# Kernel tuning notes

Measured on AMD Instinct MI355X. Metric: run time of the kernel, lower is better.

The kernel has to match this reference:

```python
import jax, jax.numpy as jnp
import numpy as np

B, S, D = 4, 2048, 1024


def setup_inputs() -> dict:
    key = jax.random.key(0)
    ks = jax.random.split(key, 9)
    scale = 1.0 / np.sqrt(D)
    q = jax.random.normal(ks[0], (B, S, D), dtype=jnp.float32)
    k = jax.random.normal(ks[1], (B, S, D), dtype=jnp.float32)
    v = jax.random.normal(ks[2], (B, S, D), dtype=jnp.float32)
    w_q = jax.random.uniform(ks[3], (D, D), jnp.float32, -scale, scale)
    b_q = jax.random.uniform(ks[4], (D,), jnp.float32, -scale, scale)
    w_k = jax.random.uniform(ks[5], (D, D), jnp.float32, -scale, scale)
    b_k = jax.random.uniform(ks[6], (D,), jnp.float32, -scale, scale)
    w_v = jax.random.uniform(ks[7], (D, D), jnp.float32, -scale, scale)
    b_v = jax.random.uniform(ks[8], (D,), jnp.float32, -scale, scale)
    # additive causal mask: 0 on/below diagonal, -1e9 above
    causal = jnp.where(jnp.tril(jnp.ones((S, S), dtype=bool)), 0.0, -1e9)
    mask = causal[None, :, :].astype(jnp.float32)  # [1, S, S]
    return {"q": q, "k": k, "v": v, "mask": mask,
            "w_q": w_q, "b_q": b_q, "w_k": w_k, "b_k": b_k,
            "w_v": w_v, "b_v": b_v}


def reference(q, k, v, mask, w_q, b_q, w_k, b_k, w_v, b_v):
    # nn.Linear: x @ W^T + b
    query = jnp.einsum('bsd,ed->bse', q, w_q) + b_q  # [B,S,D]
    key_ = jnp.einsum('bsd,ed->bse', k, w_k) + b_k
    value = jnp.einsum('bsd,ed->bse', v, w_v) + b_v
    inv_sqrt_dk = 1.0 / jnp.sqrt(jnp.asarray(D, dtype=query.dtype))
    att = jnp.einsum('bqd,bkd->bqk', query, key_) * inv_sqrt_dk  # [B,S,S]
    att = att + mask
    score = jax.nn.softmax(att, axis=-1)
    return jnp.einsum('bqk,bkd->bqd', score, value)  # [B,S,D]
```

## Files before the change

### kernel.cpp

```cpp
#include <hip/hip_runtime.h>
#include <hip/hip_bf16.h>

#define SS 2048
#define DD 1024
#define NB 4

typedef __attribute__((ext_vector_type(8))) short  bf8;
typedef __attribute__((ext_vector_type(4))) float  f32x4;

static __device__ __forceinline__ unsigned short f2bf(float f) {
    unsigned u = __float_as_uint(f);
    u += 0x7fffu + ((u >> 16) & 1u);
    return (unsigned short)(u >> 16);
}
static __device__ __forceinline__ float bf2f(unsigned short u) {
    return __uint_as_float((unsigned)u << 16);
}
static __device__ __forceinline__ unsigned short f2bf_hw(float f) {
    union { __hip_bfloat16 h; unsigned short s; } u;
    u.h = __float2bfloat16(f);
    return u.s;
}

static __device__ __forceinline__ void gload_lds16(const void* g, void* lds) {
    __builtin_amdgcn_global_load_lds((__attribute__((address_space(1))) void*)g,
                                     (__attribute__((address_space(3))) void*)lds,
                                     16, 0, 0);
}

__global__ __launch_bounds__(256)
void cvt3(const float* __restrict__ a, const float* __restrict__ b, const float* __restrict__ c,
          unsigned short* __restrict__ oa, unsigned short* __restrict__ ob,
          unsigned short* __restrict__ oc, int n4) {
    int i = blockIdx.x * 256 + threadIdx.x;
    if (i >= n4) return;
    const float* in = blockIdx.y == 0 ? a : blockIdx.y == 1 ? b : c;
    unsigned short* out = blockIdx.y == 0 ? oa : blockIdx.y == 1 ? ob : oc;
    float4 v = ((const float4*)in)[i];
    ushort4 o;
    o.x = f2bf(v.x); o.y = f2bf(v.y); o.z = f2bf(v.z); o.w = f2bf(v.w);
    ((ushort4*)out)[i] = o;
}

#define BM 128
#define BN 128
#define BK 64

template<int MODE>
__global__ __launch_bounds__(256, 2)
void gemm_bt(const void* __restrict__ A0v, const unsigned short* __restrict__ B0p,
             const float* __restrict__ bias0,
             const void* __restrict__ A1v, const unsigned short* __restrict__ B1p,
             const float* __restrict__ bias1,
             const void* __restrict__ A2v, const unsigned short* __restrict__ B2p,
             const float* __restrict__ bias2,
             void* __restrict__ Cout)
{
    constexpr int LDA = (MODE == 3) ? 2048 : 1024;
    constexpr int LDB = (MODE == 3) ? 2048 : 1024;

    int bx, by, bz;
    if (MODE == 2) {
        int f  = (int)blockIdx.x;
        int f2 = (f & 7) * 68 + (f >> 3);
        bz = f2 / 136;
        int r = f2 - bz * 136;
        by = (int)((__fsqrt_rn(8.f * (float)r + 1.f) - 1.f) * 0.5f);
        if (by > 15) by = 15;
        while ((by + 1) * (by + 2) / 2 <= r) ++by;
        while (by * (by + 1) / 2 > r) --by;
        bx = r - by * (by + 1) / 2;
    } else {
        constexpr int GX  = 8;
        constexpr int NWG = (MODE == 0) ? 512 : 192;
        constexpr int CPX = NWG >> 3;
        int f  = (int)blockIdx.y * GX + (int)blockIdx.x;
        int f2 = (f & 7) * CPX + (f >> 3);
        bx = f2 % GX; by = f2 / GX;
        bz = blockIdx.z;
    }

    const float* Af = nullptr;
    const unsigned short* Ab = nullptr;
    const unsigned short* Bm;
    const float* bias = nullptr;
    int len, qt = 0, nsp = 1;
    if (MODE == 0) {
        Af   = ((const float*)(bz == 0 ? A0v : bz == 1 ? A1v : A2v)) + (size_t)by * BM * LDA;
        Bm   = (bz == 0 ? B0p : bz == 1 ? B1p : B2p) + (size_t)bx * BN * LDB;
        bias = bz == 0 ? bias0 : bz == 1 ? bias1 : bias2;
        len  = 1024;
    } else if (MODE == 2) {
        Ab  = (const unsigned short*)A0v + (size_t)bz * SS * DD + (size_t)by * BM * LDA;
        Bm  = B0p + (size_t)bz * SS * DD + (size_t)bx * BN * LDB;
        len = 1024;
    } else {
        int seg = 0;
        if (by < 8) { qt = by; nsp = 1; }
        else        { qt = 8 + ((by - 8) >> 1); seg = (by - 8) & 1; nsp = 2; }
        int ktot = (qt + 1) * 128, hk = ktot >> 1;
        int kst  = (nsp == 2 && seg) ? hk : 0;
        len = (nsp == 1) ? ktot : hk;
        Ab = (const unsigned short*)A0v + (size_t)bz * SS * SS + (size_t)qt * BM * LDA + kst;
        Bm = B0p + (size_t)bz * DD * SS + (size_t)bx * BN * LDB + kst;
    }

    constexpr int ABYTES = (MODE == 0) ? 32768 : 16384;
    __shared__ __align__(16) char AsB[ABYTES];
    __shared__ __align__(16) unsigned short Bs[BN * BK];

    const int t = threadIdx.x;
    const int l = t & 63;
    const int w = t >> 6;
    const int wr = w >> 1, wc = w & 1;

    const int srow0 = t >> 3;
    const int sswz  = (t & 7) ^ ((t >> 3) & 7);

    f32x4 zero = {0.f, 0.f, 0.f, 0.f};
    f32x4 acc[4][4];
    #pragma unroll
    for (int i = 0; i < 4; i++)
        #pragma unroll
        for (int j = 0; j < 4; j++) acc[i][j] = zero;

    const int ar = wr * 64 + (l & 15);
    const int br = wc * 64 + (l & 15);
    const int j0 = l >> 4;

    for (int kk = 0; kk < len; kk += BK) {
        if (MODE == 0) {
            #pragma unroll
            for (int j = 0; j < 8; ++j) {
                int seg = w * 8 + j;
                int r   = seg * 4 + (l >> 4);
                int sz  = ((r & 7) << 1) | ((r >> 3) & 1);
                int cg  = (l & 15) ^ sz;
                gload_lds16(Af + (size_t)r * LDA + kk + cg * 4,
                            AsB + (size_t)(seg * 64 + l) * 16);
            }
        } else {
            #pragma unroll
            for (int j = 0; j < 4; ++j) {
                int r = srow0 + 32 * j;
                gload_lds16(Ab + (size_t)r * LDA + kk + sswz * 8,
                            AsB + (t + 256 * j) * 16);
            }
        }
        #pragma unroll
        for (int j = 0; j < 4; ++j) {
            int r = srow0 + 32 * j;
            gload_lds16(Bm + (size_t)r * LDB + kk + sswz * 8,
                        (char*)Bs + (t + 256 * j) * 16);
        }
        __syncthreads();
        #pragma unroll
        for (int ks = 0; ks < 2; ++ks) {
            bf8 af[4], bfr[4];
            #pragma unroll
            for (int i = 0; i < 4; i++) {
                int r = ar + i * 16;
                if (MODE == 0) {
                    int sz = ((r & 7) << 1) | ((r >> 3) & 1);
                    int c0 = ks * 8 + j0 * 2;
                    const char* rowb = AsB + (size_t)r * 256;
                    f32x4 lo = *(const f32x4*)(rowb + ((c0)     ^ sz) * 16);
                    f32x4 hi = *(const f32x4*)(rowb + ((c0 + 1) ^ sz) * 16);
                    bf8 vv;
                    vv[0] = (short)f2bf_hw(lo[0]); vv[1] = (short)f2bf_hw(lo[1]);
                    vv[2] = (short)f2bf_hw(lo[2]); vv[3] = (short)f2bf_hw(lo[3]);
                    vv[4] = (short)f2bf_hw(hi[0]); vv[5] = (short)f2bf_hw(hi[1]);
                    vv[6] = (short)f2bf_hw(hi[2]); vv[7] = (short)f2bf_hw(hi[3]);
                    af[i] = vv;
                } else {
                    af[i] = *(const bf8*)(AsB + (size_t)r * 128 +
                                          (((j0 + ks * 4) ^ (r & 7)) << 4));
                }
            }
            #pragma unroll
            for (int j = 0; j < 4; j++) {
                int r = br + j * 16;
                bfr[j] = *(const bf8*)((char*)Bs + (size_t)r * 128 +
                                       (((j0 + ks * 4) ^ (r & 7)) << 4));
            }
            #pragma unroll
            for (int i = 0; i < 4; i++)
                #pragma unroll
                for (int j = 0; j < 4; j++)
                    acc[i][j] = __builtin_amdgcn_mfma_f32_16x16x32_bf16(af[i], bfr[j], acc[i][j], 0, 0, 0);
        }
        __syncthreads();
    }

    const int mb = ((MODE == 3) ? qt : by) * BM + wr * 64;
    const int nb = bx * BN + wc * 64;

    if (MODE == 0) {
        float bv[4];
        #pragma unroll
        for (int j = 0; j < 4; j++) bv[j] = bias[nb + j * 16 + (l & 15)];
        if (bz < 2) {
            unsigned short* C = (unsigned short*)Cout + (size_t)bz * NB * SS * DD;
            #pragma unroll
            for (int i = 0; i < 4; i++) {
                int m0 = mb + i * 16 + ((l >> 4) << 2);
                #pragma unroll
                for (int j = 0; j < 4; j++) {
                    int n = nb + j * 16 + (l & 15);
                    #pragma unroll
                    for (int r = 0; r < 4; r++)
                        C[(size_t)(m0 + r) * DD + n] = f2bf(acc[i][j][r] + bv[j]);
                }
            }
        } else {
            unsigned short* C = (unsigned short*)Cout + (size_t)2 * NB * SS * DD;
            int batch = (by * BM) >> 11;
            #pragma unroll
            for (int i = 0; i < 4; i++) {
                int s = (mb - batch * SS) + i * 16 + ((l >> 4) << 2);
                #pragma unroll
                for (int j = 0; j < 4; j++) {
                    int n = nb + j * 16 + (l & 15);
                    ushort4 pk;
                    pk.x = f2bf(acc[i][j][0] + bv[j]);
                    pk.y = f2bf(acc[i][j][1] + bv[j]);
                    pk.z = f2bf(acc[i][j][2] + bv[j]);
                    pk.w = f2bf(acc[i][j][3] + bv[j]);
                    *(ushort4*)&C[(size_t)batch * DD * SS + (size_t)n * SS + s] = pk;
                }
            }
        }
    } else if (MODE == 2) {
        unsigned short* C = (unsigned short*)Cout + (size_t)bz * SS * SS;
        #pragma unroll
        for (int i = 0; i < 4; i++) {
            int m0 = mb + i * 16 + ((l >> 4) << 2);
            #pragma unroll
            for (int j = 0; j < 4; j++) {
                int n = nb + j * 16 + (l & 15);
                #pragma unroll
                for (int r = 0; r < 4; r++)
                    C[(size_t)(m0 + r) * SS + n] = f2bf(acc[i][j][r] * 0.03125f);
            }
        }
    } else {
        float* C = (float*)Cout + (size_t)bz * SS * DD;
        #pragma unroll
        for (int i = 0; i < 4; i++) {
            int m0 = mb + i * 16 + ((l >> 4) << 2);
            #pragma unroll
            for (int j = 0; j < 4; j++) {
                int n = nb + j * 16 + (l & 15);
                if (nsp == 1) {
                    #pragma unroll
                    for (int r = 0; r < 4; r++)
                        C[(size_t)(m0 + r) * DD + n] = acc[i][j][r];
                } else {
                    #pragma unroll
                    for (int r = 0; r < 4; r++)
                        atomicAdd(&C[(size_t)(m0 + r) * DD + n], acc[i][j][r]);
                }
            }
        }
    }
}

__global__ __launch_bounds__(256)
void softmax_causal(const unsigned short* __restrict__ Sb, unsigned short* __restrict__ P) {
    __shared__ float tm[4], tl[4];
    int row = blockIdx.x;
    int b = row >> 11, q = row & 2047;
    const unsigned short* s = Sb + ((size_t)b * SS + q) * SS;
    unsigned short* p = P + ((size_t)b * SS + q) * SS;
    int len  = q + 1;
    int len8 = len >> 3;
    int wlen = ((q >> 7) + 1) << 7;

    float m = -3e38f, lsum = 0.f;
    for (int i8 = threadIdx.x; i8 < len8; i8 += 256) {
        ushort4 u0 = ((const ushort4*)s)[i8 * 2];
        ushort4 u1 = ((const ushort4*)s)[i8 * 2 + 1];
        float v[8] = {bf2f(u0.x), bf2f(u0.y), bf2f(u0.z), bf2f(u0.w),
                      bf2f(u1.x), bf2f(u1.y), bf2f(u1.z), bf2f(u1.w)};
        float cm = v[0];
        #pragma unroll
        for (int e = 1; e < 8; ++e) cm = fmaxf(cm, v[e]);
        float cs = 0.f;
        #pragma unroll
        for (int e = 0; e < 8; ++e) cs += __expf(v[e] - cm);
        float nm = fmaxf(m, cm);
        lsum = lsum * __expf(m - nm) + cs * __expf(cm - nm);
        m = nm;
    }
    for (int i = (len8 << 3) + threadIdx.x; i < len; i += 256) {
        float v = bf2f(s[i]);
        float nm = fmaxf(m, v);
        lsum = lsum * __expf(m - nm) + __expf(v - nm);
        m = nm;
    }
    #pragma unroll
    for (int o = 32; o; o >>= 1) {
        float om = __shfl_xor(m, o);
        float ol = __shfl_xor(lsum, o);
        float nm = fmaxf(m, om);
        lsum = lsum * __expf(m - nm) + ol * __expf(om - nm);
        m = nm;
    }
    if ((threadIdx.x & 63) == 0) { tm[threadIdx.x >> 6] = m; tl[threadIdx.x >> 6] = lsum; }
    __syncthreads();
    {
        float gm = fmaxf(fmaxf(tm[0], tm[1]), fmaxf(tm[2], tm[3]));
        float gl = tl[0] * __expf(tm[0] - gm) + tl[1] * __expf(tm[1] - gm)
                 + tl[2] * __expf(tm[2] - gm) + tl[3] * __expf(tm[3] - gm);
        m = gm; lsum = gl;
    }
    float inv = 1.f / lsum;

    for (int i8 = threadIdx.x; i8 < (wlen >> 3); i8 += 256) {
        int i = i8 << 3;
        ushort4 u0 = ((const ushort4*)s)[i8 * 2];
        ushort4 u1 = ((const ushort4*)s)[i8 * 2 + 1];
        ushort4 o0, o1;
        o0.x = (i     < len) ? f2bf(__expf(bf2f(u0.x) - m) * inv) : (unsigned short)0;
        o0.y = (i + 1 < len) ? f2bf(__expf(bf2f(u0.y) - m) * inv) : (unsigned short)0;
        o0.z = (i + 2 < len) ? f2bf(__expf(bf2f(u0.z) - m) * inv) : (unsigned short)0;
        o0.w = (i + 3 < len) ? f2bf(__expf(bf2f(u0.w) - m) * inv) : (unsigned short)0;
        o1.x = (i + 4 < len) ? f2bf(__expf(bf2f(u1.x) - m) * inv) : (unsigned short)0;
        o1.y = (i + 5 < len) ? f2bf(__expf(bf2f(u1.y) - m) * inv) : (unsigned short)0;
        o1.z = (i + 6 < len) ? f2bf(__expf(bf2f(u1.z) - m) * inv) : (unsigned short)0;
        o1.w = (i + 7 < len) ? f2bf(__expf(bf2f(u1.w) - m) * inv) : (unsigned short)0;
        ((ushort4*)p)[i8 * 2]     = o0;
        ((ushort4*)p)[i8 * 2 + 1] = o1;
    }
}

extern "C" void kernel_launch(void* const* d_in, const int* in_sizes, int n_in,
                              void* d_out, int out_size, void* d_ws, size_t ws_size,
                              hipStream_t stream) {
    constexpr size_t NX = (size_t)NB * SS * DD;
    constexpr size_t NW = (size_t)DD * DD;

    const float* q   = (const float*)d_in[0];
    const float* k   = (const float*)d_in[1];
    const float* v   = (const float*)d_in[2];
    const float* w_q = (const float*)d_in[4];
    const float* b_q = (const float*)d_in[5];
    const float* w_k = (const float*)d_in[6];
    const float* b_k = (const float*)d_in[7];
    const float* w_v = (const float*)d_in[8];
    const float* b_v = (const float*)d_in[9];
    float* out = (float*)d_out;

    char* ws = (char*)d_ws;
    size_t off = 0;
    auto take = [&](size_t bytes) { char* p = ws + off; off += (bytes + 255) & ~(size_t)255; return p; };
    unsigned short* wqb = (unsigned short*)take(NW * 2);
    unsigned short* wkb = (unsigned short*)take(NW * 2);
    unsigned short* wvb = (unsigned short*)take(NW * 2);
    unsigned short* QKV = (unsigned short*)take(NX * 2 * 3);
    unsigned short* Sb  = (unsigned short*)take((size_t)NB * SS * SS * 2);
    unsigned short* P   = (unsigned short*)take((size_t)NB * SS * SS * 2);
    unsigned short* Qp  = QKV;
    unsigned short* Kp  = QKV + NX;
    unsigned short* VpT = QKV + 2 * NX;

    dim3 blk(256);
    for (int b = 0; b < NB; ++b)
        hipMemsetAsync(out + ((size_t)b * SS + 1024) * DD, 0, (size_t)1024 * DD * 4, stream);
    cvt3<<<dim3(NW / 4 / 256, 3), blk, 0, stream>>>(w_q, w_k, w_v, wqb, wkb, wvb, (int)(NW / 4));

    gemm_bt<0><<<dim3(8, 64, 3), blk, 0, stream>>>(
        q, wqb, b_q, k, wkb, b_k, v, wvb, b_v, QKV);

    gemm_bt<2><<<dim3(544), blk, 0, stream>>>(
        Qp, Kp, nullptr, nullptr, nullptr, nullptr, nullptr, nullptr, nullptr, Sb);

    softmax_causal<<<dim3(NB * SS), blk, 0, stream>>>(Sb, P);

    gemm_bt<3><<<dim3(8, 24, 4), blk, 0, stream>>>(
        P, VpT, nullptr, nullptr, nullptr, nullptr, nullptr, nullptr, nullptr, out);
}
```

Measured before the change: 176.8 us.

## Schedule PV GEMM tiles via packed lookup tables and raise occupancy hint

```diff
diff --git a/kernel.cpp b/kernel.cpp
--- a/kernel.cpp
+++ b/kernel.cpp
@@ -47,7 +47,7 @@
 #define BK 64
 
 template<int MODE>
-__global__ __launch_bounds__(256, 2)
+__global__ __launch_bounds__(256, 3)
 void gemm_bt(const void* __restrict__ A0v, const unsigned short* __restrict__ B0p,
              const float* __restrict__ bias0,
              const void* __restrict__ A1v, const unsigned short* __restrict__ B1p,
@@ -60,6 +60,7 @@
     constexpr int LDB = (MODE == 3) ? 2048 : 1024;
 
     int bx, by, bz;
+    int qt = 0, nsp = 1, seg = 0;
     if (MODE == 2) {
         int f  = (int)blockIdx.x;
         int f2 = (f & 7) * 68 + (f >> 3);
@@ -70,10 +71,27 @@
         while ((by + 1) * (by + 2) / 2 <= r) ++by;
         while (by * (by + 1) / 2 > r) --by;
         bx = r - by * (by + 1) / 2;
+    } else if (MODE == 3) {
+        constexpr unsigned long long T0 = 7ull | 63ull << 6 | 46ull << 12 | 62ull << 18 |
+                                          45ull << 24 | 61ull << 30 | 60ull << 36 | 43ull << 42;
+        constexpr unsigned long long T1 = 47ull | 6ull << 6 | 44ull << 12 | 42ull << 18 |
+                                          4ull << 24 | 58ull << 30 | 5ull << 36 | 59ull << 42;
+        constexpr unsigned long long T2 = 0ull | 1ull << 6 | 2ull << 12 | 3ull << 18 |
+                                          41ull << 24 | 40ull << 30 | 56ull << 36 | 57ull << 42;
+        int f = (int)blockIdx.x;
+        int layer = f >> 8, ti = f & 255;
+        bz = ti >> 6;
+        bx = (ti >> 3) & 7;
+        int t = ti & 7;
+        unsigned long long tab = layer == 0 ? T0 : layer == 1 ? T1 : T2;
+        int e = (int)((tab >> (t * 6)) & 63);
+        qt  = e & 15;
+        seg = (e >> 4) & 1;
+        nsp = ((e >> 5) & 1) ? 2 : 1;
+        by  = 0;
     } else {
         constexpr int GX  = 8;
-        constexpr int NWG = (MODE == 0) ? 512 : 192;
-        constexpr int CPX = NWG >> 3;
+        constexpr int CPX = 512 >> 3;
         int f  = (int)blockIdx.y * GX + (int)blockIdx.x;
         int f2 = (f & 7) * CPX + (f >> 3);
         bx = f2 % GX; by = f2 / GX;
@@ -84,7 +102,7 @@
     const unsigned short* Ab = nullptr;
     const unsigned short* Bm;
     const float* bias = nullptr;
-    int len, qt = 0, nsp = 1;
+    int len;
     if (MODE == 0) {
         Af   = ((const float*)(bz == 0 ? A0v : bz == 1 ? A1v : A2v)) + (size_t)by * BM * LDA;
         Bm   = (bz == 0 ? B0p : bz == 1 ? B1p : B2p) + (size_t)bx * BN * LDB;
@@ -95,9 +113,6 @@
         Bm  = B0p + (size_t)bz * SS * DD + (size_t)bx * BN * LDB;
         len = 1024;
     } else {
-        int seg = 0;
-        if (by < 8) { qt = by; nsp = 1; }
-        else        { qt = 8 + ((by - 8) >> 1); seg = (by - 8) & 1; nsp = 2; }
         int ktot = (qt + 1) * 128, hk = ktot >> 1;
         int kst  = (nsp == 2 && seg) ? hk : 0;
         len = (nsp == 1) ? ktot : hk;
@@ -132,12 +147,12 @@
         if (MODE == 0) {
             #pragma unroll
             for (int j = 0; j < 8; ++j) {
-                int seg = w * 8 + j;
-                int r   = seg * 4 + (l >> 4);
-                int sz  = ((r & 7) << 1) | ((r >> 3) & 1);
-                int cg  = (l & 15) ^ sz;
+                int sg = w * 8 + j;
+                int r  = sg * 4 + (l >> 4);
+                int sz = ((r & 7) << 1) | ((r >> 3) & 1);
+                int cg = (l & 15) ^ sz;
                 gload_lds16(Af + (size_t)r * LDA + kk + cg * 4,
-                            AsB + (size_t)(seg * 64 + l) * 16);
+                            AsB + (size_t)(sg * 64 + l) * 16);
             }
         } else {
             #pragma unroll
@@ -377,6 +392,6 @@
 
     softmax_causal<<<dim3(NB * SS), blk, 0, stream>>>(Sb, P);
 
-    gemm_bt<3><<<dim3(8, 24, 4), blk, 0, stream>>>(
+    gemm_bt<3><<<dim3(768), blk, 0, stream>>>(
         P, VpT, nullptr, nullptr, nullptr, nullptr, nullptr, nullptr, nullptr, out);
 }
```

Measured after the change: 176.2 us (median of 2 runs). No clear change (-0.3%).
